# Kernel tuning notes

Measured on AMD Instinct MI355X. Metric: run time of the kernel, lower is better.

## Reference

```python
import jax, jax.numpy as jnp
import numpy as np

N_NODES = 50000
N_EDGES = 800000
HIDDEN = 128
NUM_LAYERS = 3
NEG_SLOPE = 0.2  # PyG GATConv default leaky_relu slope


def setup_inputs() -> dict:
    key = jax.random.key(0)
    ks = jax.random.split(key, 10)
    d = HIDDEN
    glorot = 1.0 / np.sqrt(d)
    inp = {
        "x": jax.random.normal(ks[0], (N_NODES, d), dtype=jnp.float32),
        "edge_index": jax.random.randint(ks[1], (2, N_EDGES), 0, N_NODES, dtype=jnp.int32),
        "edge_mask": jax.random.uniform(ks[2], (N_EDGES,), dtype=jnp.float32),
        # GATConv params (heads=1)
        "W_gat": jax.random.normal(ks[3], (d, d), dtype=jnp.float32) * glorot,
        "a_src": jax.random.normal(ks[4], (d,), dtype=jnp.float32) * glorot,
        "a_dst": jax.random.normal(ks[5], (d,), dtype=jnp.float32) * glorot,
        "b_gat": jnp.zeros((d,), dtype=jnp.float32),
        # Stacked GCNConv params
        "W_gcn": jax.random.normal(ks[6], (NUM_LAYERS, d, d), dtype=jnp.float32) * glorot,
        "b_gcn": jnp.zeros((NUM_LAYERS, d), dtype=jnp.float32),
    }
    return inp


def _seg_softmax(e, seg, n):
    m = jax.ops.segment_max(e, seg, num_segments=n)
    p = jnp.exp(e - m[seg])
    s = jax.ops.segment_sum(p, seg, num_segments=n)
    return p / s[seg]


def reference(x, edge_index, edge_mask, W_gat, a_src, a_dst, b_gat, W_gcn, b_gcn):
    N = x.shape[0]
    loops = jnp.arange(N, dtype=edge_index.dtype)
    src = jnp.concatenate([edge_index[0], loops])  # [E+N] with self loops
    dst = jnp.concatenate([edge_index[1], loops])

    # --- GATConv (heads=1, add_self_loops=True); edge_attr ignored (edge_dim=None) ---
    xp = x @ W_gat                                      # [N, d]
    e = jax.nn.leaky_relu((xp @ a_src)[src] + (xp @ a_dst)[dst], NEG_SLOPE)
    alpha = _seg_softmax(e, dst, N)                     # segment softmax over incoming edges
    h = jax.ops.segment_sum(alpha[:, None] * xp[src], dst, num_segments=N) + b_gat

    # --- GCN normalization with edge_mask as edge_weight (self-loop weight = 1) ---
    w = jnp.concatenate([edge_mask, jnp.ones((N,), dtype=edge_mask.dtype)])
    deg = jax.ops.segment_sum(w, dst, num_segments=N)
    dinv = jnp.where(deg > 0, jax.lax.rsqrt(jnp.maximum(deg, 1e-12)), 0.0)
    norm = dinv[src] * w * dinv[dst]                    # [E+N]

    outs = [h]
    for l in range(NUM_LAYERS):
        z = outs[-1] @ W_gcn[l]                         # [N, d]
        z = jax.ops.segment_sum(norm[:, None] * z[src], dst, num_segments=N) + b_gcn[l]
        outs.append(jax.nn.relu(z))

    # JumpingKnowledge 'max': elementwise max over layer outputs
    return jnp.max(jnp.stack(outs, axis=0), axis=0)
```

## Files before the change

### kernel.cpp

```cpp
#include <hip/hip_runtime.h>

#define HIDDEN 128
#define NEG_SLOPE 0.2f
#define P_SORT 256

typedef unsigned short ushort_t;
typedef __attribute__((ext_vector_type(8))) short short8;
typedef __attribute__((ext_vector_type(4))) float floatx4;

static inline size_t align_up(size_t x, size_t a){ return (x + a - 1) & ~(a - 1); }

__device__ __forceinline__ ushort_t f2b(float f){
  unsigned u = __float_as_uint(f);
  unsigned r = (u + 0x7FFFu + ((u >> 16) & 1u)) >> 16;
  return (ushort_t)r;
}

__device__ __forceinline__ void fma8(float* acc, uint4 v, float a){
  acc[0] += a * __uint_as_float(v.x << 16);
  acc[1] += a * __uint_as_float(v.x & 0xFFFF0000u);
  acc[2] += a * __uint_as_float(v.y << 16);
  acc[3] += a * __uint_as_float(v.y & 0xFFFF0000u);
  acc[4] += a * __uint_as_float(v.z << 16);
  acc[5] += a * __uint_as_float(v.z & 0xFFFF0000u);
  acc[6] += a * __uint_as_float(v.w << 16);
  acc[7] += a * __uint_as_float(v.w & 0xFFFF0000u);
}

__device__ __forceinline__ uint4 pack8(const float* f){
  uint4 u;
  u.x = (unsigned)f2b(f[0]) | ((unsigned)f2b(f[1]) << 16);
  u.y = (unsigned)f2b(f[2]) | ((unsigned)f2b(f[3]) << 16);
  u.z = (unsigned)f2b(f[4]) | ((unsigned)f2b(f[5]) << 16);
  u.w = (unsigned)f2b(f[6]) | ((unsigned)f2b(f[7]) << 16);
  return u;
}


__global__ __launch_bounds__(256) void k_b1cnt(const int* __restrict__ dst,
                                               int* __restrict__ bcnt,
                                               int E, int epb, int nbkt){
  __shared__ unsigned c[256];
  int t = threadIdx.x;
  c[t] = 0;
  __syncthreads();
  int e0 = blockIdx.x * epb;
  int e1 = min(E, e0 + epb);
  for (int e = e0 + t; e < e1; e += 256) atomicAdd(&c[dst[e] >> 8], 1u);
  __syncthreads();
  if (t < nbkt) bcnt[t * P_SORT + blockIdx.x] = (int)c[t];
}

__global__ void k_scan1(const int* __restrict__ in, int* __restrict__ incl,
                        int* __restrict__ blockSums, int M){
  __shared__ int sd[256];
  int t = threadIdx.x;
  int i = blockIdx.x*256 + t;
  int v = (i < M) ? in[i] : 0;
  sd[t] = v; __syncthreads();
  for (int off = 1; off < 256; off <<= 1){
    int add = (t >= off) ? sd[t-off] : 0;
    __syncthreads();
    sd[t] += add;
    __syncthreads();
  }
  if (i < M) incl[i] = sd[t];
  if (t == 255) blockSums[blockIdx.x] = sd[255];
}

__global__ void k_scan2(const int* __restrict__ blockSums, int* __restrict__ blockOffs, int nb){
  __shared__ int sd[256];
  __shared__ int carry;
  int t = threadIdx.x;
  if (t == 0) carry = 0;
  __syncthreads();
  for (int base = 0; base < nb; base += 256){
    int i = base + t;
    int v = (i < nb) ? blockSums[i] : 0;
    sd[t] = v; __syncthreads();
    for (int off = 1; off < 256; off <<= 1){
      int add = (t >= off) ? sd[t-off] : 0;
      __syncthreads();
      sd[t] += add;
      __syncthreads();
    }
    if (i < nb) blockOffs[i] = carry + sd[t] - v;
    __syncthreads();
    if (t == 0) carry += sd[255];
    __syncthreads();
  }
}

__global__ __launch_bounds__(256) void k_b1place(const int* __restrict__ src,
                                                 const int* __restrict__ dst,
                                                 const float* __restrict__ w,
                                                 const int* __restrict__ incl,
                                                 const int* __restrict__ bcnt,
                                                 const int* __restrict__ blockOffs,
                                                 int2* __restrict__ tpw,
                                                 int E, int epb, int nbkt){
  __shared__ int base_[256];
  __shared__ unsigned c[256];
  int t = threadIdx.x;
  c[t] = 0;
  if (t < nbkt){
    int idx = t * P_SORT + blockIdx.x;
    base_[t] = incl[idx] - bcnt[idx] + blockOffs[t];
  }
  __syncthreads();
  int e0 = blockIdx.x * epb;
  int e1 = min(E, e0 + epb);
  for (int e = e0 + t; e < e1; e += 256){
    int d = dst[e];
    int b = d >> 8;
    unsigned r = atomicAdd(&c[b], 1u);
    int pos = base_[b] + (int)r;
    tpw[pos] = make_int2((int)((unsigned)src[e] | ((unsigned)(d & 255) << 16)),
                         __float_as_int(w[e]));
  }
}

__global__ __launch_bounds__(256) void k_b2(const int2* __restrict__ tpw,
                                            const int* __restrict__ blockOffs,
                                            int2* __restrict__ col_sw,
                                            int* __restrict__ rowp,
                                            float* __restrict__ dinv,
                                            int N, int E, int nbkt){
  __shared__ int cnt[4096];
  __shared__ int tsum[256];
  __shared__ float wsum[256];
  int b = blockIdx.x, t = threadIdx.x;
  int e0 = blockOffs[b];
  int e1 = (b + 1 < nbkt) ? blockOffs[b + 1] : E;
  #pragma unroll
  for (int i = 0; i < 16; i++) cnt[t*16 + i] = 0;
  wsum[t] = 0.f;
  __syncthreads();
  for (int e = e0 + t; e < e1; e += 256){
    int2 pw = tpw[e];
    unsigned dl = ((unsigned)pw.x >> 16) & 255u;
    unsigned s  = ((unsigned)pw.x & 0xFFFFu) >> 12;
    atomicAdd(&cnt[(dl << 4) | s], 1);
  }
  __syncthreads();
  int loc[16]; int run = 0;
  #pragma unroll
  for (int i = 0; i < 16; i++){ loc[i] = run; run += cnt[t*16 + i]; }
  tsum[t] = run;
  __syncthreads();
  for (int off = 1; off < 256; off <<= 1){
    int add = (t >= off) ? tsum[t-off] : 0;
    __syncthreads();
    tsum[t] += add;
    __syncthreads();
  }
  int base = tsum[t] - run;
  #pragma unroll
  for (int i = 0; i < 16; i++) cnt[t*16 + i] = base + loc[i];
  int node = b*256 + t;
  if (node < N) rowp[node] = e0 + base;
  if (b == 0 && t == 0) rowp[N] = E;
  __syncthreads();
  for (int e = e0 + t; e < e1; e += 256){
    int2 pw = tpw[e];
    unsigned dl = ((unsigned)pw.x >> 16) & 255u;
    unsigned srcv = (unsigned)pw.x & 0xFFFFu;
    unsigned s = srcv >> 12;
    int pos = e0 + atomicAdd(&cnt[(dl << 4) | s], 1);
    col_sw[pos] = make_int2((int)srcv, pw.y);
    atomicAdd(&wsum[dl], __int_as_float(pw.y));
  }
  __syncthreads();
  if (node < N) dinv[node] = rsqrtf(wsum[t] + 1.0f);
}


__global__ void k_cast_w(const float* __restrict__ Wg, const float* __restrict__ Wc,
                         ushort_t* __restrict__ Wt){
  int i = blockIdx.x*256 + threadIdx.x;
  int mat = i >> 14, idx = i & 16383;
  int k = idx >> 7, n = idx & 127;
  float v = (mat == 0) ? Wg[idx] : Wc[(mat-1)*16384 + idx];
  Wt[mat*16384 + n*128 + k] = f2b(v);
}

template<int DOTS>
__global__ __launch_bounds__(256) void k_gemm(const void* __restrict__ Ain,
                                              const ushort_t* __restrict__ Wt,
                                              ushort_t* __restrict__ C,
                                              const float* __restrict__ a_src,
                                              const float* __restrict__ a_dst,
                                              const float* __restrict__ dinv,
                                              float2* __restrict__ attr,
                                              float* __restrict__ sdst, int M){
  int wave = threadIdx.x >> 6, l = threadIdx.x & 63;
  int q = l >> 4, lm = l & 15;
  int rowBase = blockIdx.x*128 + wave*32;
  floatx4 acc[2][8];
  #pragma unroll
  for (int mt = 0; mt < 2; mt++)
    #pragma unroll
    for (int nt = 0; nt < 8; nt++) acc[mt][nt] = (floatx4){0.f,0.f,0.f,0.f};

  #pragma unroll
  for (int kc = 0; kc < 4; kc++){
    int k0 = kc*32 + q*8;
    short8 a[2];
    #pragma unroll
    for (int mt = 0; mt < 2; mt++){
      long r = rowBase + mt*16 + lm;
      if (r < M){
        if (DOTS){
          const float* ap = (const float*)Ain + r*128 + k0;
          float4 u = *(const float4*)ap;
          float4 v = *(const float4*)(ap + 4);
          short8 tv;
          tv[0]=(short)f2b(u.x); tv[1]=(short)f2b(u.y); tv[2]=(short)f2b(u.z); tv[3]=(short)f2b(u.w);
          tv[4]=(short)f2b(v.x); tv[5]=(short)f2b(v.y); tv[6]=(short)f2b(v.z); tv[7]=(short)f2b(v.w);
          a[mt] = tv;
        } else {
          a[mt] = *(const short8*)((const ushort_t*)Ain + r*128 + k0);
        }
      } else a[mt] = (short8){0,0,0,0,0,0,0,0};
    }
    #pragma unroll
    for (int nt = 0; nt < 8; nt++){
      short8 b = *(const short8*)(Wt + (nt*16 + lm)*128 + k0);
      acc[0][nt] = __builtin_amdgcn_mfma_f32_16x16x32_bf16(a[0], b, acc[0][nt], 0, 0, 0);
      acc[1][nt] = __builtin_amdgcn_mfma_f32_16x16x32_bf16(a[1], b, acc[1][nt], 0, 0, 0);
    }
  }
  #pragma unroll
  for (int mt = 0; mt < 2; mt++){
    #pragma unroll
    for (int r = 0; r < 4; r++){
      long row = rowBase + mt*16 + q*4 + r;
      if (row < M){
        #pragma unroll
        for (int nt = 0; nt < 8; nt++)
          C[row*128 + nt*16 + lm] = f2b(acc[mt][nt][r]);
      }
    }
  }
  if (DOTS){
    float as8[8], ad8[8];
    #pragma unroll
    for (int nt = 0; nt < 8; nt++){ as8[nt] = a_src[nt*16 + lm]; ad8[nt] = a_dst[nt*16 + lm]; }
    #pragma unroll
    for (int mt = 0; mt < 2; mt++){
      #pragma unroll
      for (int r = 0; r < 4; r++){
        float ps = 0.f, pd = 0.f;
        #pragma unroll
        for (int nt = 0; nt < 8; nt++){
          ps += acc[mt][nt][r] * as8[nt];
          pd += acc[mt][nt][r] * ad8[nt];
        }
        #pragma unroll
        for (int off = 1; off <= 8; off <<= 1){
          ps += __shfl_xor(ps, off, 64);
          pd += __shfl_xor(pd, off, 64);
        }
        long row = rowBase + mt*16 + q*4 + r;
        if (lm == 0 && row < M){
          attr[row] = make_float2(ps, dinv[row]);
          sdst[row] = pd;
        }
      }
    }
  }
}

template<int MODE>
__global__ __launch_bounds__(256) void k_agg(const ushort_t* __restrict__ feat,
                                             const int* __restrict__ rowp,
                                             const int2* __restrict__ col_sw,
                                             int2* __restrict__ col_en,
                                             int2* __restrict__ col_ea,
                                             const float2* __restrict__ attr,
                                             const float* __restrict__ sdst_,
                                             const float* __restrict__ dinv,
                                             const float* __restrict__ bias,
                                             ushort_t* __restrict__ out,
                                             const uint4* __restrict__ j0,
                                             const uint4* __restrict__ j1,
                                             const uint4* __restrict__ j2,
                                             float4* __restrict__ yout, int N){
  int n = blockIdx.x*4 + (threadIdx.x >> 6);
  if (n >= N) return;
  int l = threadIdx.x & 63;
  int rs = rowp[n], re = rowp[n+1];
  float inv = 0.f, pself = 0.f;
  if (MODE == 0){
    float2 an = attr[n];
    float sdd = sdst_[n];
    float es = an.x + sdd;
    es = (es >= 0.f) ? es : NEG_SLOPE*es;
    pself = __expf(es);
    float ps = 0.f;
    for (int j = rs + l; j < re; j += 64){
      int2 sw = col_sw[j];
      float w = __int_as_float(sw.y);
      float2 a = attr[sw.x];
      col_en[j] = make_int2(sw.x, __float_as_int(a.y * w * an.y));
      float ee = a.x + sdd;
      ee = (ee >= 0.f) ? ee : NEG_SLOPE*ee;
      float pe = __expf(ee);
      ps += pe;
      col_ea[j] = make_int2(sw.x, __float_as_int(pe));
    }
    #pragma unroll
    for (int off = 32; off >= 1; off >>= 1) ps += __shfl_xor(ps, off, 64);
    inv = 1.f / (ps + pself);
  }
  const int2* col = (MODE == 0) ? (const int2*)col_ea : (const int2*)col_en;
  int sub = l >> 4, q = l & 15;
  const uint4* f16 = (const uint4*)feat;
  float acc[8] = {0.f,0.f,0.f,0.f,0.f,0.f,0.f,0.f};
  for (int base = rs; base < re; base += 24){
    int2 p[6]; float a[6];
    #pragma unroll
    for (int j = 0; j < 6; j++){
      int e = base + sub + 4*j;
      int cc = min(e, re-1);
      p[j] = col[cc];
      a[j] = (e < re) ? __int_as_float(p[j].y) : 0.f;
    }
    uint4 v[6];
    #pragma unroll
    for (int j = 0; j < 6; j++) v[j] = f16[(size_t)p[j].x*16 + q];
    #pragma unroll
    for (int j = 0; j < 6; j++) fma8(acc, v[j], a[j]);
  }
  #pragma unroll
  for (int j = 0; j < 8; j++){
    acc[j] += __shfl_xor(acc[j], 16, 64);
    acc[j] += __shfl_xor(acc[j], 32, 64);
  }
  if (sub == 0){
    float sc;
    if (MODE == 0){
      #pragma unroll
      for (int j = 0; j < 8; j++) acc[j] *= inv;
      sc = pself * inv;
    } else {
      float di = dinv[n];
      sc = di * di;
    }
    uint4 v = f16[(size_t)n*16 + q];
    fma8(acc, v, sc);
    float4 b0 = ((const float4*)bias)[q*2];
    float4 b1 = ((const float4*)bias)[q*2 + 1];
    acc[0]+=b0.x; acc[1]+=b0.y; acc[2]+=b0.z; acc[3]+=b0.w;
    acc[4]+=b1.x; acc[5]+=b1.y; acc[6]+=b1.z; acc[7]+=b1.w;
    if (MODE >= 1){
      #pragma unroll
      for (int j = 0; j < 8; j++) acc[j] = fmaxf(acc[j], 0.f);
    }
    if (MODE <= 1){
      ((uint4*)out)[(size_t)n*16 + q] = pack8(acc);
    } else {
      size_t qi = (size_t)n*16 + q;
      uint4 a0 = j0[qi], a1 = j1[qi], a2 = j2[qi];
      float m[8];
      #pragma unroll
      for (int k = 0; k < 4; k++){
        unsigned u0 = (&a0.x)[k], u1 = (&a1.x)[k], u2 = (&a2.x)[k];
        float lo = fmaxf(fmaxf(__uint_as_float(u0 << 16), __uint_as_float(u1 << 16)),
                         __uint_as_float(u2 << 16));
        float hi = fmaxf(fmaxf(__uint_as_float(u0 & 0xFFFF0000u), __uint_as_float(u1 & 0xFFFF0000u)),
                         __uint_as_float(u2 & 0xFFFF0000u));
        m[k*2]   = fmaxf(acc[k*2],   lo);
        m[k*2+1] = fmaxf(acc[k*2+1], hi);
      }
      size_t yi = (size_t)n*32 + q*2;
      yout[yi]   = make_float4(m[0], m[1], m[2], m[3]);
      yout[yi+1] = make_float4(m[4], m[5], m[6], m[7]);
    }
  }
}

extern "C" void kernel_launch(void* const* d_in, const int* in_sizes, int n_in,
                              void* d_out, int out_size, void* d_ws, size_t ws_size,
                              hipStream_t stream){
  const float* x      = (const float*)d_in[0];
  const int*   eidx   = (const int*)d_in[1];
  const float* emask  = (const float*)d_in[2];
  const float* W_gat  = (const float*)d_in[3];
  const float* a_src  = (const float*)d_in[4];
  const float* a_dst  = (const float*)d_in[5];
  const float* b_gat  = (const float*)d_in[6];
  const float* W_gcn  = (const float*)d_in[7];
  const float* b_gcn  = (const float*)d_in[8];
  int N = in_sizes[0] / HIDDEN;
  int E = in_sizes[1] / 2;
  const int* src = eidx;
  const int* dst = eidx + E;

  char* p = (char*)d_ws;
  auto carve = [&](size_t bytes)->char*{ char* q = p; p += align_up(bytes, 512); return q; };
  ushort_t* zb   = (ushort_t*)carve((size_t)N*HIDDEN*2);
  ushort_t* h0   = (ushort_t*)carve((size_t)N*HIDDEN*2);
  ushort_t* h1   = (ushort_t*)carve((size_t)N*HIDDEN*2);
  ushort_t* h2   = (ushort_t*)carve((size_t)N*HIDDEN*2);
  ushort_t* Wt   = (ushort_t*)carve((size_t)4*HIDDEN*HIDDEN*2);
  float2* attr   = (float2*)carve((size_t)N*8);
  float* sdst    = (float*)carve((size_t)N*4);
  float* dinv    = (float*)carve((size_t)N*4);
  int*   rowp    = (int*)  carve((size_t)(N+1)*4);
  int2*  col_sw  = (int2*) carve((size_t)E*8);
  int2*  col_en  = (int2*) carve((size_t)E*8);
  int2*  col_ea  = (int2*) carve((size_t)E*8);
  int2*  tpw     = (int2*) carve((size_t)E*8);
  int nbkt = (N + 255) >> 8;
  int M    = nbkt * P_SORT;
  int*   bcnt  = (int*)carve((size_t)M*4);
  int*   incl  = (int*)carve((size_t)M*4);
  int nbs = (M + 255) / 256;
  int*   blockSums = (int*)carve((size_t)nbs*4);
  int*   blockOffs = (int*)carve((size_t)nbs*4);
  (void)ws_size; (void)n_in; (void)out_size;

  int epb = (E + P_SORT - 1) / P_SORT;
  int gb  = (N + 127) / 128;
  int nwb = (N + 3) / 4;

  k_b1cnt  <<<P_SORT, 256, 0, stream>>>(dst, bcnt, E, epb, nbkt);
  k_scan1  <<<nbs, 256, 0, stream>>>(bcnt, incl, blockSums, M);
  k_scan2  <<<1,   256, 0, stream>>>(blockSums, blockOffs, nbs);
  k_b1place<<<P_SORT, 256, 0, stream>>>(src, dst, emask, incl, bcnt, blockOffs,
                                        tpw, E, epb, nbkt);
  k_b2     <<<nbkt, 256, 0, stream>>>(tpw, blockOffs, col_sw, rowp, dinv, N, E, nbkt);

  k_cast_w<<<(4*HIDDEN*HIDDEN)/256, 256, 0, stream>>>(W_gat, W_gcn, Wt);

  k_gemm<1><<<gb, 256, 0, stream>>>((const void*)x, Wt, zb, a_src, a_dst, dinv, attr, sdst, N);

  k_agg<0><<<nwb, 256, 0, stream>>>(zb, rowp, col_sw, col_en, col_ea, attr, sdst,
                                    dinv, b_gat, h0, nullptr, nullptr, nullptr, nullptr, N);

  ushort_t* hs[3] = {h0, h1, h2};
  for (int l = 0; l < 2; l++){
    k_gemm<0><<<gb, 256, 0, stream>>>((const void*)hs[l], Wt + (size_t)(l+1)*HIDDEN*HIDDEN,
                                      zb, a_src, a_dst, dinv, attr, sdst, N);
    k_agg<1><<<nwb, 256, 0, stream>>>(zb, rowp, col_sw, col_en, col_ea, attr, sdst,
                                      dinv, b_gcn + (size_t)l*HIDDEN, hs[l+1],
                                      nullptr, nullptr, nullptr, nullptr, N);
  }
  k_gemm<0><<<gb, 256, 0, stream>>>((const void*)h2, Wt + (size_t)3*HIDDEN*HIDDEN,
                                    zb, a_src, a_dst, dinv, attr, sdst, N);
  k_agg<2><<<nwb, 256, 0, stream>>>(zb, rowp, col_sw, col_en, col_ea, attr, sdst,
                                    dinv, b_gcn + (size_t)2*HIDDEN, nullptr,
                                    (const uint4*)h0, (const uint4*)h1, (const uint4*)h2,
                                    (float4*)d_out, N);
}
```

Before: 347.4 us.

## Reorder GCN layers to aggregate-then-transform and fuse the GEMM into aggregation

Uses the identity A(hW) = (Ah)W to aggregate bf16 node features first, then runs a small MFMA GEMM on a 16-row tile held in shared memory inside the same kernel. This fuses the three GCN layers' separate gemm and agg launches into single kernels and removes the zb intermediate round-trip. It also shrinks the GAT gemm block to 64 rows. The cost is an extra bf16 rounding of the aggregated features before the matmul, less work per block for the gather phase, and JK outputs written as scalar stores instead of vectorized ones.

```diff
diff --git a/kernel.cpp b/kernel.cpp
--- a/kernel.cpp
+++ b/kernel.cpp
@@ -14,6 +14,10 @@
   unsigned u = __float_as_uint(f);
   unsigned r = (u + 0x7FFFu + ((u >> 16) & 1u)) >> 16;
   return (ushort_t)r;
+}
+
+__device__ __forceinline__ float b2f(ushort_t u){
+  return __uint_as_float(((unsigned)u) << 16);
 }
 
 __device__ __forceinline__ void fma8(float* acc, uint4 v, float a){
@@ -184,18 +188,17 @@
   Wt[mat*16384 + n*128 + k] = f2b(v);
 }
 
-template<int DOTS>
-__global__ __launch_bounds__(256) void k_gemm(const void* __restrict__ Ain,
-                                              const ushort_t* __restrict__ Wt,
-                                              ushort_t* __restrict__ C,
-                                              const float* __restrict__ a_src,
-                                              const float* __restrict__ a_dst,
-                                              const float* __restrict__ dinv,
-                                              float2* __restrict__ attr,
-                                              float* __restrict__ sdst, int M){
+__global__ __launch_bounds__(128) void k_gemm1(const float* __restrict__ Ain,
+                                               const ushort_t* __restrict__ Wt,
+                                               ushort_t* __restrict__ C,
+                                               const float* __restrict__ a_src,
+                                               const float* __restrict__ a_dst,
+                                               const float* __restrict__ dinv,
+                                               float2* __restrict__ attr,
+                                               float* __restrict__ sdst, int M){
   int wave = threadIdx.x >> 6, l = threadIdx.x & 63;
   int q = l >> 4, lm = l & 15;
-  int rowBase = blockIdx.x*128 + wave*32;
+  int rowBase = blockIdx.x*64 + wave*32;
   floatx4 acc[2][8];
   #pragma unroll
   for (int mt = 0; mt < 2; mt++)
@@ -210,17 +213,13 @@
     for (int mt = 0; mt < 2; mt++){
       long r = rowBase + mt*16 + lm;
       if (r < M){
-        if (DOTS){
-          const float* ap = (const float*)Ain + r*128 + k0;
-          float4 u = *(const float4*)ap;
-          float4 v = *(const float4*)(ap + 4);
-          short8 tv;
-          tv[0]=(short)f2b(u.x); tv[1]=(short)f2b(u.y); tv[2]=(short)f2b(u.z); tv[3]=(short)f2b(u.w);
-          tv[4]=(short)f2b(v.x); tv[5]=(short)f2b(v.y); tv[6]=(short)f2b(v.z); tv[7]=(short)f2b(v.w);
-          a[mt] = tv;
-        } else {
-          a[mt] = *(const short8*)((const ushort_t*)Ain + r*128 + k0);
-        }
+        const float* ap = Ain + r*128 + k0;
+        float4 u = *(const float4*)ap;
+        float4 v = *(const float4*)(ap + 4);
+        short8 tv;
+        tv[0]=(short)f2b(u.x); tv[1]=(short)f2b(u.y); tv[2]=(short)f2b(u.z); tv[3]=(short)f2b(u.w);
+        tv[4]=(short)f2b(v.x); tv[5]=(short)f2b(v.y); tv[6]=(short)f2b(v.z); tv[7]=(short)f2b(v.w);
+        a[mt] = tv;
       } else a[mt] = (short8){0,0,0,0,0,0,0,0};
     }
     #pragma unroll
@@ -242,78 +241,67 @@
       }
     }
   }
-  if (DOTS){
-    float as8[8], ad8[8];
-    #pragma unroll
-    for (int nt = 0; nt < 8; nt++){ as8[nt] = a_src[nt*16 + lm]; ad8[nt] = a_dst[nt*16 + lm]; }
-    #pragma unroll
-    for (int mt = 0; mt < 2; mt++){
+  float as8[8], ad8[8];
+  #pragma unroll
+  for (int nt = 0; nt < 8; nt++){ as8[nt] = a_src[nt*16 + lm]; ad8[nt] = a_dst[nt*16 + lm]; }
+  #pragma unroll
+  for (int mt = 0; mt < 2; mt++){
+    #pragma unroll
+    for (int r = 0; r < 4; r++){
+      float ps = 0.f, pd = 0.f;
       #pragma unroll
-      for (int r = 0; r < 4; r++){
-        float ps = 0.f, pd = 0.f;
-        #pragma unroll
-        for (int nt = 0; nt < 8; nt++){
-          ps += acc[mt][nt][r] * as8[nt];
-          pd += acc[mt][nt][r] * ad8[nt];
-        }
-        #pragma unroll
-        for (int off = 1; off <= 8; off <<= 1){
-          ps += __shfl_xor(ps, off, 64);
-          pd += __shfl_xor(pd, off, 64);
-        }
-        long row = rowBase + mt*16 + q*4 + r;
-        if (lm == 0 && row < M){
-          attr[row] = make_float2(ps, dinv[row]);
-          sdst[row] = pd;
-        }
-      }
-    }
-  }
-}
-
-template<int MODE>
-__global__ __launch_bounds__(256) void k_agg(const ushort_t* __restrict__ feat,
-                                             const int* __restrict__ rowp,
-                                             const int2* __restrict__ col_sw,
-                                             int2* __restrict__ col_en,
-                                             int2* __restrict__ col_ea,
-                                             const float2* __restrict__ attr,
-                                             const float* __restrict__ sdst_,
-                                             const float* __restrict__ dinv,
-                                             const float* __restrict__ bias,
-                                             ushort_t* __restrict__ out,
-                                             const uint4* __restrict__ j0,
-                                             const uint4* __restrict__ j1,
-                                             const uint4* __restrict__ j2,
-                                             float4* __restrict__ yout, int N){
+      for (int nt = 0; nt < 8; nt++){
+        ps += acc[mt][nt][r] * as8[nt];
+        pd += acc[mt][nt][r] * ad8[nt];
+      }
+      #pragma unroll
+      for (int off = 1; off <= 8; off <<= 1){
+        ps += __shfl_xor(ps, off, 64);
+        pd += __shfl_xor(pd, off, 64);
+      }
+      long row = rowBase + mt*16 + q*4 + r;
+      if (lm == 0 && row < M){
+        attr[row] = make_float2(ps, dinv[row]);
+        sdst[row] = pd;
+      }
+    }
+  }
+}
+
+__global__ __launch_bounds__(256) void k_agg0(const ushort_t* __restrict__ feat,
+                                              const int* __restrict__ rowp,
+                                              const int2* __restrict__ col_sw,
+                                              int2* __restrict__ col_en,
+                                              int2* __restrict__ col_ea,
+                                              const float2* __restrict__ attr,
+                                              const float* __restrict__ sdst_,
+                                              const float* __restrict__ bias,
+                                              ushort_t* __restrict__ out, int N){
   int n = blockIdx.x*4 + (threadIdx.x >> 6);
   if (n >= N) return;
   int l = threadIdx.x & 63;
   int rs = rowp[n], re = rowp[n+1];
-  float inv = 0.f, pself = 0.f;
-  if (MODE == 0){
-    float2 an = attr[n];
-    float sdd = sdst_[n];
-    float es = an.x + sdd;
-    es = (es >= 0.f) ? es : NEG_SLOPE*es;
-    pself = __expf(es);
-    float ps = 0.f;
-    for (int j = rs + l; j < re; j += 64){
-      int2 sw = col_sw[j];
-      float w = __int_as_float(sw.y);
-      float2 a = attr[sw.x];
-      col_en[j] = make_int2(sw.x, __float_as_int(a.y * w * an.y));
-      float ee = a.x + sdd;
-      ee = (ee >= 0.f) ? ee : NEG_SLOPE*ee;
-      float pe = __expf(ee);
-      ps += pe;
-      col_ea[j] = make_int2(sw.x, __float_as_int(pe));
-    }
-    #pragma unroll
-    for (int off = 32; off >= 1; off >>= 1) ps += __shfl_xor(ps, off, 64);
-    inv = 1.f / (ps + pself);
-  }
-  const int2* col = (MODE == 0) ? (const int2*)col_ea : (const int2*)col_en;
+  float2 an = attr[n];
+  float sdd = sdst_[n];
+  float es = an.x + sdd;
+  es = (es >= 0.f) ? es : NEG_SLOPE*es;
+  float pself = __expf(es);
+  float ps = 0.f;
+  for (int j = rs + l; j < re; j += 64){
+    int2 sw = col_sw[j];
+    float w = __int_as_float(sw.y);
+    float2 a = attr[sw.x];
+    col_en[j] = make_int2(sw.x, __float_as_int(a.y * w * an.y));
+    float ee = a.x + sdd;
+    ee = (ee >= 0.f) ? ee : NEG_SLOPE*ee;
+    float pe = __expf(ee);
+    ps += pe;
+    col_ea[j] = make_int2(sw.x, __float_as_int(pe));
+  }
+  #pragma unroll
+  for (int off = 32; off >= 1; off >>= 1) ps += __shfl_xor(ps, off, 64);
+  float inv = 1.f / (ps + pself);
+
   int sub = l >> 4, q = l & 15;
   const uint4* f16 = (const uint4*)feat;
   float acc[8] = {0.f,0.f,0.f,0.f,0.f,0.f,0.f,0.f};
@@ -323,7 +311,7 @@
     for (int j = 0; j < 6; j++){
       int e = base + sub + 4*j;
       int cc = min(e, re-1);
-      p[j] = col[cc];
+      p[j] = col_ea[cc];
       a[j] = (e < re) ? __int_as_float(p[j].y) : 0.f;
     }
     uint4 v[6];
@@ -338,44 +326,106 @@
     acc[j] += __shfl_xor(acc[j], 32, 64);
   }
   if (sub == 0){
-    float sc;
-    if (MODE == 0){
-      #pragma unroll
-      for (int j = 0; j < 8; j++) acc[j] *= inv;
-      sc = pself * inv;
-    } else {
-      float di = dinv[n];
-      sc = di * di;
-    }
+    #pragma unroll
+    for (int j = 0; j < 8; j++) acc[j] *= inv;
     uint4 v = f16[(size_t)n*16 + q];
-    fma8(acc, v, sc);
+    fma8(acc, v, pself * inv);
     float4 b0 = ((const float4*)bias)[q*2];
     float4 b1 = ((const float4*)bias)[q*2 + 1];
     acc[0]+=b0.x; acc[1]+=b0.y; acc[2]+=b0.z; acc[3]+=b0.w;
     acc[4]+=b1.x; acc[5]+=b1.y; acc[6]+=b1.z; acc[7]+=b1.w;
-    if (MODE >= 1){
+    ((uint4*)out)[(size_t)n*16 + q] = pack8(acc);
+  }
+}
+
+template<int MODE>
+__global__ __launch_bounds__(256) void k_fagg(const ushort_t* __restrict__ feat,
+                                              const int* __restrict__ rowp,
+                                              const int2* __restrict__ col_en,
+                                              const float* __restrict__ dinv,
+                                              const ushort_t* __restrict__ Wl,
+                                              const float* __restrict__ bias,
+                                              ushort_t* __restrict__ out,
+                                              const ushort_t* __restrict__ j0,
+                                              const ushort_t* __restrict__ j1,
+                                              const ushort_t* __restrict__ j2,
+                                              float* __restrict__ yout, int N){
+  __shared__ ushort_t At[16][136];
+  int wave = threadIdx.x >> 6, l = threadIdx.x & 63;
+  int sub = l >> 4, q = l & 15;
+  const uint4* f16 = (const uint4*)feat;
+  int tile = blockIdx.x * 16;
+
+  for (int i = 0; i < 4; i++){
+    int row = wave*4 + i;
+    int n = tile + row;
+    int rs = 0, re = 0;
+    if (n < N){ rs = rowp[n]; re = rowp[n+1]; }
+    float acc[8] = {0.f,0.f,0.f,0.f,0.f,0.f,0.f,0.f};
+    for (int base = rs; base < re; base += 24){
+      int2 p[6]; float a[6];
       #pragma unroll
-      for (int j = 0; j < 8; j++) acc[j] = fmaxf(acc[j], 0.f);
-    }
-    if (MODE <= 1){
-      ((uint4*)out)[(size_t)n*16 + q] = pack8(acc);
-    } else {
-      size_t qi = (size_t)n*16 + q;
-      uint4 a0 = j0[qi], a1 = j1[qi], a2 = j2[qi];
-      float m[8];
+      for (int j = 0; j < 6; j++){
+        int e = base + sub + 4*j;
+        int cc = min(e, re-1);
+        p[j] = col_en[cc];
+        a[j] = (e < re) ? __int_as_float(p[j].y) : 0.f;
+      }
+      uint4 v[6];
       #pragma unroll
-      for (int k = 0; k < 4; k++){
-        unsigned u0 = (&a0.x)[k], u1 = (&a1.x)[k], u2 = (&a2.x)[k];
-        float lo = fmaxf(fmaxf(__uint_as_float(u0 << 16), __uint_as_float(u1 << 16)),
-                         __uint_as_float(u2 << 16));
-        float hi = fmaxf(fmaxf(__uint_as_float(u0 & 0xFFFF0000u), __uint_as_float(u1 & 0xFFFF0000u)),
-                         __uint_as_float(u2 & 0xFFFF0000u));
-        m[k*2]   = fmaxf(acc[k*2],   lo);
-        m[k*2+1] = fmaxf(acc[k*2+1], hi);
-      }
-      size_t yi = (size_t)n*32 + q*2;
-      yout[yi]   = make_float4(m[0], m[1], m[2], m[3]);
-      yout[yi+1] = make_float4(m[4], m[5], m[6], m[7]);
+      for (int j = 0; j < 6; j++) v[j] = f16[(size_t)p[j].x*16 + q];
+      #pragma unroll
+      for (int j = 0; j < 6; j++) fma8(acc, v[j], a[j]);
+    }
+    #pragma unroll
+    for (int j = 0; j < 8; j++){
+      acc[j] += __shfl_xor(acc[j], 16, 64);
+      acc[j] += __shfl_xor(acc[j], 32, 64);
+    }
+    if (sub == 0){
+      if (n < N){
+        float di = dinv[n];
+        uint4 v = f16[(size_t)n*16 + q];
+        fma8(acc, v, di*di);
+      }
+      *(uint4*)&At[row][q*8] = pack8(acc);
+    }
+  }
+  __syncthreads();
+
+  floatx4 co[2];
+  co[0] = (floatx4){0.f,0.f,0.f,0.f};
+  co[1] = (floatx4){0.f,0.f,0.f,0.f};
+  #pragma unroll
+  for (int kc = 0; kc < 4; kc++){
+    int k0 = kc*32 + sub*8;
+    short8 a = *(const short8*)&At[q][k0];
+    #pragma unroll
+    for (int ntl = 0; ntl < 2; ntl++){
+      int nt = wave*2 + ntl;
+      short8 b = *(const short8*)(Wl + (size_t)(nt*16 + q)*128 + k0);
+      co[ntl] = __builtin_amdgcn_mfma_f32_16x16x32_bf16(a, b, co[ntl], 0, 0, 0);
+    }
+  }
+  #pragma unroll
+  for (int r = 0; r < 4; r++){
+    int row = sub*4 + r;
+    int node = tile + row;
+    if (node < N){
+      #pragma unroll
+      for (int ntl = 0; ntl < 2; ntl++){
+        int colg = wave*32 + ntl*16 + q;
+        float v = co[ntl][r] + bias[colg];
+        v = fmaxf(v, 0.f);
+        size_t idx = (size_t)node*128 + colg;
+        if (MODE == 1){
+          out[idx] = f2b(v);
+        } else {
+          float m = fmaxf(fmaxf(b2f(j0[idx]), b2f(j1[idx])),
+                          fmaxf(b2f(j2[idx]), v));
+          yout[idx] = m;
+        }
+      }
     }
   }
 }
@@ -422,8 +472,9 @@
   (void)ws_size; (void)n_in; (void)out_size;
 
   int epb = (E + P_SORT - 1) / P_SORT;
-  int gb  = (N + 127) / 128;
+  int gb  = (N + 63) / 64;
   int nwb = (N + 3) / 4;
+  int nfb = (N + 15) / 16;
 
   k_b1cnt  <<<P_SORT, 256, 0, stream>>>(dst, bcnt, E, epb, nbkt);
   k_scan1  <<<nbs, 256, 0, stream>>>(bcnt, incl, blockSums, M);
@@ -434,23 +485,18 @@
 
   k_cast_w<<<(4*HIDDEN*HIDDEN)/256, 256, 0, stream>>>(W_gat, W_gcn, Wt);
 
-  k_gemm<1><<<gb, 256, 0, stream>>>((const void*)x, Wt, zb, a_src, a_dst, dinv, attr, sdst, N);
-
-  k_agg<0><<<nwb, 256, 0, stream>>>(zb, rowp, col_sw, col_en, col_ea, attr, sdst,
-                                    dinv, b_gat, h0, nullptr, nullptr, nullptr, nullptr, N);
-
-  ushort_t* hs[3] = {h0, h1, h2};
-  for (int l = 0; l < 2; l++){
-    k_gemm<0><<<gb, 256, 0, stream>>>((const void*)hs[l], Wt + (size_t)(l+1)*HIDDEN*HIDDEN,
-                                      zb, a_src, a_dst, dinv, attr, sdst, N);
-    k_agg<1><<<nwb, 256, 0, stream>>>(zb, rowp, col_sw, col_en, col_ea, attr, sdst,
-                                      dinv, b_gcn + (size_t)l*HIDDEN, hs[l+1],
-                                      nullptr, nullptr, nullptr, nullptr, N);
-  }
-  k_gemm<0><<<gb, 256, 0, stream>>>((const void*)h2, Wt + (size_t)3*HIDDEN*HIDDEN,
-                                    zb, a_src, a_dst, dinv, attr, sdst, N);
-  k_agg<2><<<nwb, 256, 0, stream>>>(zb, rowp, col_sw, col_en, col_ea, attr, sdst,
-                                    dinv, b_gcn + (size_t)2*HIDDEN, nullptr,
-                                    (const uint4*)h0, (const uint4*)h1, (const uint4*)h2,
-                                    (float4*)d_out, N);
-}
+  k_gemm1<<<gb, 128, 0, stream>>>(x, Wt, zb, a_src, a_dst, dinv, attr, sdst, N);
+
+  k_agg0<<<nwb, 256, 0, stream>>>(zb, rowp, col_sw, col_en, col_ea, attr, sdst,
+                                  b_gat, h0, N);
+
+  k_fagg<1><<<nfb, 256, 0, stream>>>(h0, rowp, col_en, dinv, Wt + (size_t)1*16384,
+                                     b_gcn + 0, h1,
+                                     nullptr, nullptr, nullptr, nullptr, N);
+  k_fagg<1><<<nfb, 256, 0, stream>>>(h1, rowp, col_en, dinv, Wt + (size_t)2*16384,
+                                     b_gcn + 128, h2,
+                                     nullptr, nullptr, nullptr, nullptr, N);
+  k_fagg<2><<<nfb, 256, 0, stream>>>(h2, rowp, col_en, dinv, Wt + (size_t)3*16384,
+                                     b_gcn + 256, nullptr,
+                                     h0, h1, h2, (float*)d_out, N);
+}
```

Result: faster. 340.6 us (-2.0%).
